# Kernel tuning notes

Hardware: AMD Instinct MI355X
Metric: run time of the kernel (lower is better)

The kernel has to match this reference:

```python
import jax, jax.numpy as jnp
import numpy as np

DIM = 1024
NUM_HEADS = 16
HEAD_DIM = DIM // NUM_HEADS


def setup_inputs() -> dict:
    key = jax.random.key(0)
    k1, k2, k3, k4, k5, k6 = jax.random.split(key, 6)
    B, T, C = 4, 2048, DIM
    s = 1.0 / np.sqrt(C)
    return {
        "x": jax.random.normal(k1, (B, T, C), dtype=jnp.float32),
        "attn_bias": jax.random.normal(k2, (B, T, T), dtype=jnp.float32),
        "qkv_w": jax.random.uniform(k3, (3 * C, C), dtype=jnp.float32, minval=-s, maxval=s),
        "qkv_b": jax.random.uniform(k4, (3 * C,), dtype=jnp.float32, minval=-s, maxval=s),
        "out_w": jax.random.uniform(k5, (C, C), dtype=jnp.float32, minval=-s, maxval=s),
        "out_b": jax.random.uniform(k6, (C,), dtype=jnp.float32, minval=-s, maxval=s),
    }


def reference(x, attn_bias, qkv_w, qkv_b, out_w, out_b):
    B, T, C = x.shape
    H, D = NUM_HEADS, HEAD_DIM
    # fused QKV projection (torch Linear: x @ W^T + b)
    qkv = jnp.einsum('btc,fc->btf', x, qkv_w) + qkv_b  # [B,T,3C]
    q, k, v = jnp.split(qkv, 3, axis=-1)
    q = q.reshape(B, T, H, D).transpose(0, 2, 1, 3)  # [B,H,T,D]
    k = k.reshape(B, T, H, D).transpose(0, 2, 1, 3)
    v = v.reshape(B, T, H, D).transpose(0, 2, 1, 3)
    scores = jnp.einsum('bhtd,bhsd->bhts', q, k) / jnp.sqrt(jnp.float32(D))
    scores = scores + attn_bias[:, None, :, :]  # 3-D bias -> broadcast over heads
    attn = jax.nn.softmax(scores, axis=-1)
    out = jnp.einsum('bhts,bhsd->bhtd', attn, v)  # [B,H,T,D]
    out = out.transpose(0, 2, 1, 3).reshape(B, T, C)
    return jnp.einsum('btc,fc->btf', out, out_w) + out_b
```

## Files before the change

### kernel.cpp

```cpp
#include <hip/hip_runtime.h>

#define BATCH 4
#define SEQ   2048
#define CDIM  1024
#define HEADS 16
#define HDIM  64
#define N3    3072
#define NTOK  8192
#define QKP   2048
#define LOG2E 1.44269504f

typedef __attribute__((ext_vector_type(4))) float    float4v;
typedef __attribute__((ext_vector_type(8))) short    short8;
typedef __attribute__((ext_vector_type(8))) __bf16   bf16x8;
typedef __attribute__((ext_vector_type(4))) _Float16 half4v;
typedef __attribute__((ext_vector_type(2))) _Float16 half2v;

__device__ __forceinline__ unsigned short f2bf(float f) {
    union { float f; unsigned int u; } x; x.f = f;
    unsigned int r = x.u + 0x7fffu + ((x.u >> 16) & 1u);
    return (unsigned short)(r >> 16);
}

__device__ __forceinline__ bf16x8 ld_bf8(const unsigned short* p) {
    short8 s = *(const short8*)p;
    return __builtin_bit_cast(bf16x8, s);
}

__device__ __forceinline__ void glds16(const void* g, void* l) {
    __builtin_amdgcn_global_load_lds(
        (const __attribute__((address_space(1))) void*)g,
        (__attribute__((address_space(3))) void*)l, 16, 0, 0);
}

__global__ void cast_f32_bf16(const float* __restrict__ in,
                              unsigned short* __restrict__ out, int n4) {
    int i = blockIdx.x * blockDim.x + threadIdx.x;
    if (i >= n4) return;
    float4v v = ((const float4v*)in)[i];
    ushort4 r;
    r.x = f2bf(v[0]); r.y = f2bf(v[1]); r.z = f2bf(v[2]); r.w = f2bf(v[3]);
    ((ushort4*)out)[i] = r;
}

__global__ __launch_bounds__(256, 3)
void gemm_bt(const unsigned short* __restrict__ A,
             const unsigned short* __restrict__ Bm,
             const float* __restrict__ bias,
             void* __restrict__ Cout,
             void* __restrict__ Cout2,
             int M, int N, int K, int mode)
{
    __shared__ alignas(16) unsigned short As[128 * 64];
    __shared__ alignas(16) unsigned short Bs[128 * 64];

    const int tid  = threadIdx.x;
    const int lane = tid & 63;
    const int wave = tid >> 6;
    const int wr = wave >> 1, wc = wave & 1;
    const int lm = lane & 15, quad = lane >> 4;
    const size_t m0 = (size_t)blockIdx.y * 128;
    const size_t n0 = (size_t)blockIdx.x * 128;

    const unsigned short* ag[4];
    const unsigned short* bg[4];
    unsigned short* la[4];
    unsigned short* lb[4];
#pragma unroll
    for (int i = 0; i < 4; i++) {
        int idx = tid + i * 256;
        int row = idx >> 3;
        int lc  = (idx & 7) ^ (row & 7);
        ag[i] = &A [(m0 + row) * K + lc * 8];
        bg[i] = &Bm[(n0 + row) * K + lc * 8];
        la[i] = &As[(idx & ~63) * 8];
        lb[i] = &Bs[(idx & ~63) * 8];
    }

    float4v acc[4][4];
#pragma unroll
    for (int i = 0; i < 4; i++)
#pragma unroll
        for (int j = 0; j < 4; j++) acc[i][j] = (float4v){0.f, 0.f, 0.f, 0.f};

    for (int k0 = 0; k0 < K; k0 += 64) {
#pragma unroll
        for (int i = 0; i < 4; i++) glds16(ag[i], la[i]);
#pragma unroll
        for (int i = 0; i < 4; i++) glds16(bg[i], lb[i]);
#pragma unroll
        for (int i = 0; i < 4; i++) { ag[i] += 64; bg[i] += 64; }
        __syncthreads();
#pragma unroll
        for (int kk = 0; kk < 2; kk++) {
            bf16x8 af[4], bfr[4];
#pragma unroll
            for (int t = 0; t < 4; t++) {
                int slot = ((quad + kk * 4) ^ (lm & 7)) * 8;
                af [t] = ld_bf8(&As[(wr * 64 + t * 16 + lm) * 64 + slot]);
                bfr[t] = ld_bf8(&Bs[(wc * 64 + t * 16 + lm) * 64 + slot]);
            }
#pragma unroll
            for (int ti = 0; ti < 4; ti++)
#pragma unroll
                for (int tj = 0; tj < 4; tj++)
                    acc[ti][tj] = __builtin_amdgcn_mfma_f32_16x16x32_bf16(
                        af[ti], bfr[tj], acc[ti][tj], 0, 0, 0);
        }
        __syncthreads();
    }

#pragma unroll
    for (int ti = 0; ti < 4; ti++) {
        size_t row = m0 + wr * 64 + ti * 16 + quad * 4;
#pragma unroll
        for (int tj = 0; tj < 4; tj++) {
            int col = (int)n0 + wc * 64 + tj * 16 + lm;
            float bv = bias[col];
            if (mode == 0) {
#pragma unroll
                for (int r = 0; r < 4; r++)
                    ((float*)Cout)[(row + r) * N + col] = acc[ti][tj][r] + bv;
            } else if (col < 2 * CDIM) {
#pragma unroll
                for (int r = 0; r < 4; r++)
                    ((unsigned short*)Cout)[(row + r) * QKP + col] =
                        f2bf(acc[ti][tj][r] + bv);
            } else {
                int hd = col - 2 * CDIM;
                int bb = (int)(row >> 11);
                int s  = (int)(row & 2047);
                half4v hv;
#pragma unroll
                for (int r = 0; r < 4; r++) hv[r] = (_Float16)(acc[ti][tj][r] + bv);
                *(half4v*)((unsigned short*)Cout2 +
                           ((size_t)bb * CDIM + hd) * SEQ + s) = hv;
            }
        }
    }
}

__global__ __launch_bounds__(256, 4)
void attn_kernel(const unsigned short* __restrict__ qk,
                 const unsigned short* __restrict__ vT,
                 const float* __restrict__ bias,
                 unsigned short* __restrict__ outp)
{
    __shared__ alignas(16) char smem[32768];
    float*          BiasS = (float*)smem;
    unsigned short* Qs    = (unsigned short*)smem;
    unsigned short* Ks    = (unsigned short*)(smem + 16384);
    unsigned short* Vts   = (unsigned short*)(smem + 24576);

    const int tid  = threadIdx.x;
    const int lane = tid & 63, wave = tid >> 6;
    const int lm = lane & 15, quad = lane >> 4;
    const int q0 = blockIdx.x * 64;
    const int bh = blockIdx.y;
    const int bb = bh >> 4, h = bh & 15;
    const size_t rowbase = (size_t)bb * SEQ;
    const unsigned short* vTh = vT + (size_t)bh * HDIM * SEQ;
    const float* biasb = bias + (size_t)bb * SEQ * SEQ + (size_t)q0 * SEQ;

#pragma unroll
    for (int i = 0; i < 2; i++) {
        int idx = tid + i * 256;
        int row = idx >> 3;
        int lc  = (idx & 7) ^ (row & 7);
        glds16(&qk[(rowbase + q0 + row) * QKP + h * 64 + lc * 8], &Qs[(idx & ~63) * 8]);
    }
    __syncthreads();
    bf16x8 bq[2];
#pragma unroll
    for (int kk = 0; kk < 2; kk++)
        bq[kk] = ld_bf8(&Qs[(wave * 16 + lm) * 64 + (((quad + kk * 4) ^ (lm & 7)) * 8)]);

    const unsigned short *kg0, *kg1, *vg0, *vg1;
    unsigned short *lk0, *lk1, *lv0, *lv1;
    {
        int idx = tid, row = idx >> 3, lc = (idx & 7) ^ (row & 7);
        kg0 = &qk[(rowbase + row) * QKP + CDIM + h * 64 + lc * 8];
        vg0 = &vTh[(size_t)row * SEQ + lc * 8];
        lk0 = &Ks[(idx & ~63) * 8];
        lv0 = &Vts[(idx & ~63) * 8];
        idx = tid + 256; row = idx >> 3; lc = (idx & 7) ^ (row & 7);
        kg1 = &qk[(rowbase + row) * QKP + CDIM + h * 64 + lc * 8];
        vg1 = &vTh[(size_t)row * SEQ + lc * 8];
        lk1 = &Ks[(idx & ~63) * 8];
        lv1 = &Vts[(idx & ~63) * 8];
    }
    const float* bgp[4];
    float*       lbp[4];
#pragma unroll
    for (int i = 0; i < 4; i++) {
        int idx = tid + i * 256;
        int row = idx >> 4;
        int lc  = (idx & 15) ^ (row & 15);
        bgp[i] = &biasb[(size_t)row * SEQ + lc * 4];
        lbp[i] = &BiasS[(idx & ~63) * 4];
    }

    float rsum = 0.f;
    float4v o[4];
#pragma unroll
    for (int t = 0; t < 4; t++) o[t] = (float4v){0.f, 0.f, 0.f, 0.f};

    for (int it = 0; it < SEQ / 64; ++it) {
        __syncthreads();
        glds16(kg0, lk0); glds16(kg1, lk1);
        glds16(vg0, lv0); glds16(vg1, lv1);
#pragma unroll
        for (int i = 0; i < 4; i++) glds16(bgp[i], lbp[i]);
        kg0 += 64 * QKP; kg1 += 64 * QKP;
        vg0 += 64; vg1 += 64;
#pragma unroll
        for (int i = 0; i < 4; i++) bgp[i] += 64;
        __syncthreads();

        float4v st[4];
#pragma unroll
        for (int tj = 0; tj < 4; tj++) {
            bf16x8 ak0 = ld_bf8(&Ks[(tj * 16 + lm) * 64 + (((quad    ) ^ (lm & 7)) * 8)]);
            bf16x8 ak1 = ld_bf8(&Ks[(tj * 16 + lm) * 64 + (((quad + 4) ^ (lm & 7)) * 8)]);
            st[tj] = (float4v){0.f, 0.f, 0.f, 0.f};
            st[tj] = __builtin_amdgcn_mfma_f32_16x16x32_bf16(ak0, bq[0], st[tj], 0, 0, 0);
            st[tj] = __builtin_amdgcn_mfma_f32_16x16x32_bf16(ak1, bq[1], st[tj], 0, 0, 0);
        }

        half4v pa[4];
#pragma unroll
        for (int tj = 0; tj < 4; tj++) {
            float4v bv = *(const float4v*)&BiasS[(wave * 16 + lm) * 64 +
                                                 (((tj * 4 + quad) ^ lm) * 4)];
            float p[4];
#pragma unroll
            for (int r = 0; r < 4; r++) {
                float sc = fmaf(st[tj][r], 0.125f, bv[r]);
                p[r] = exp2f(sc * LOG2E);
                rsum += p[r];
            }
            half2v plo = __builtin_bit_cast(half2v, __builtin_amdgcn_cvt_pkrtz(p[0], p[1]));
            half2v phi = __builtin_bit_cast(half2v, __builtin_amdgcn_cvt_pkrtz(p[2], p[3]));
            pa[tj][0] = plo[0]; pa[tj][1] = plo[1];
            pa[tj][2] = phi[0]; pa[tj][3] = phi[1];
        }

#pragma unroll
        for (int tj = 0; tj < 4; tj++) {
            int c = tj * 4 + quad;
#pragma unroll
            for (int dt = 0; dt < 4; dt++) {
                int row = dt * 16 + lm;
                int off = (((c >> 1) ^ (lm & 7)) * 8) + (c & 1) * 4;
                half4v vb = *(const half4v*)&Vts[row * 64 + off];
                o[dt] = __builtin_amdgcn_mfma_f32_16x16x16f16(pa[tj], vb, o[dt], 0, 0, 0);
            }
        }
    }

    float l = rsum;
    l += __shfl_xor(l, 16);
    l += __shfl_xor(l, 32);
    float invl = 1.0f / l;
    float i4[4];
#pragma unroll
    for (int r = 0; r < 4; r++) i4[r] = __shfl(invl, quad * 4 + r, 16);
#pragma unroll
    for (int dt = 0; dt < 4; dt++) {
        int col = h * 64 + dt * 16 + lm;
#pragma unroll
        for (int r = 0; r < 4; r++) {
            size_t trow = rowbase + q0 + wave * 16 + quad * 4 + r;
            outp[trow * CDIM + col] = f2bf(o[dt][r] * i4[r]);
        }
    }
}

extern "C" void kernel_launch(void* const* d_in, const int* in_sizes, int n_in,
                              void* d_out, int out_size, void* d_ws, size_t ws_size,
                              hipStream_t stream)
{
    const float* x         = (const float*)d_in[0];
    const float* attn_bias = (const float*)d_in[1];
    const float* qkv_w     = (const float*)d_in[2];
    const float* qkv_b     = (const float*)d_in[3];
    const float* out_w     = (const float*)d_in[4];
    const float* out_b     = (const float*)d_in[5];
    float* out = (float*)d_out;

    char* p = (char*)d_ws;
    unsigned short* x_bf   = (unsigned short*)p; p += (size_t)NTOK * CDIM * 2;
    unsigned short* wq_bf  = (unsigned short*)p; p += (size_t)N3 * CDIM * 2;
    unsigned short* wo_bf  = (unsigned short*)p; p += (size_t)CDIM * CDIM * 2;
    unsigned short* qk_bf  = (unsigned short*)p; p += (size_t)NTOK * QKP * 2;
    unsigned short* vT_f16 = (unsigned short*)p; p += (size_t)BATCH * CDIM * SEQ * 2;
    unsigned short* at_bf  = (unsigned short*)p;

    int n4;
    n4 = NTOK * CDIM / 4;
    cast_f32_bf16<<<(n4 + 255) / 256, 256, 0, stream>>>(x, x_bf, n4);
    n4 = N3 * CDIM / 4;
    cast_f32_bf16<<<(n4 + 255) / 256, 256, 0, stream>>>(qkv_w, wq_bf, n4);
    n4 = CDIM * CDIM / 4;
    cast_f32_bf16<<<(n4 + 255) / 256, 256, 0, stream>>>(out_w, wo_bf, n4);

    gemm_bt<<<dim3(N3 / 128, NTOK / 128), 256, 0, stream>>>(
        x_bf, wq_bf, qkv_b, qk_bf, vT_f16, NTOK, N3, CDIM, 1);

    attn_kernel<<<dim3(SEQ / 64, BATCH * HEADS), 256, 0, stream>>>(
        qk_bf, vT_f16, attn_bias, at_bf);

    gemm_bt<<<dim3(CDIM / 128, NTOK / 128), 256, 0, stream>>>(
        at_bf, wo_bf, out_b, out, nullptr, NTOK, CDIM, CDIM, 0);
}
```

Before: 363.7 us.

## Fold softmax scale into Q, seed MFMA with bias, compute row sums via MFMA

The QKV GEMM epilogue now multiplies Q by scale*log2e, so the attention kernel seeds the QK^T MFMA accumulator with bias*log2e and applies raw exp2 directly to the result. This drops the per-element FMA and multiply. The per-lane scalar row-sum accumulation and the cross-lane shuffles are replaced by an extra MFMA against a ones vector, which yields the row sums already in the output layout. This adds four MFMAs per tile and stores pre-scaled Q in bf16, which changes rounding slightly.

```diff
diff --git a/kernel.cpp b/kernel.cpp
--- a/kernel.cpp
+++ b/kernel.cpp
@@ -9,6 +9,7 @@
 #define NTOK  8192
 #define QKP   2048
 #define LOG2E 1.44269504f
+#define QSC   0.18033688f
 
 typedef __attribute__((ext_vector_type(4))) float    float4v;
 typedef __attribute__((ext_vector_type(8))) short    short8;
@@ -122,10 +123,11 @@
                 for (int r = 0; r < 4; r++)
                     ((float*)Cout)[(row + r) * N + col] = acc[ti][tj][r] + bv;
             } else if (col < 2 * CDIM) {
+                float scl = (col < CDIM) ? QSC : 1.0f;
 #pragma unroll
                 for (int r = 0; r < 4; r++)
                     ((unsigned short*)Cout)[(row + r) * QKP + col] =
-                        f2bf(acc[ti][tj][r] + bv);
+                        f2bf((acc[ti][tj][r] + bv) * scl);
             } else {
                 int hd = col - 2 * CDIM;
                 int bb = (int)(row >> 11);
@@ -200,7 +202,8 @@
         lbp[i] = &BiasS[(idx & ~63) * 4];
     }
 
-    float rsum = 0.f;
+    const half4v vones = {(_Float16)1.f, (_Float16)1.f, (_Float16)1.f, (_Float16)1.f};
+    float4v rs4 = (float4v){0.f, 0.f, 0.f, 0.f};
     float4v o[4];
 #pragma unroll
     for (int t = 0; t < 4; t++) o[t] = (float4v){0.f, 0.f, 0.f, 0.f};
@@ -220,9 +223,11 @@
         float4v st[4];
 #pragma unroll
         for (int tj = 0; tj < 4; tj++) {
+            float4v bv = *(const float4v*)&BiasS[(wave * 16 + lm) * 64 +
+                                                 (((tj * 4 + quad) ^ lm) * 4)];
+            st[tj] = bv * LOG2E;
             bf16x8 ak0 = ld_bf8(&Ks[(tj * 16 + lm) * 64 + (((quad    ) ^ (lm & 7)) * 8)]);
             bf16x8 ak1 = ld_bf8(&Ks[(tj * 16 + lm) * 64 + (((quad + 4) ^ (lm & 7)) * 8)]);
-            st[tj] = (float4v){0.f, 0.f, 0.f, 0.f};
             st[tj] = __builtin_amdgcn_mfma_f32_16x16x32_bf16(ak0, bq[0], st[tj], 0, 0, 0);
             st[tj] = __builtin_amdgcn_mfma_f32_16x16x32_bf16(ak1, bq[1], st[tj], 0, 0, 0);
         }
@@ -230,20 +235,19 @@
         half4v pa[4];
 #pragma unroll
         for (int tj = 0; tj < 4; tj++) {
-            float4v bv = *(const float4v*)&BiasS[(wave * 16 + lm) * 64 +
-                                                 (((tj * 4 + quad) ^ lm) * 4)];
-            float p[4];
-#pragma unroll
-            for (int r = 0; r < 4; r++) {
-                float sc = fmaf(st[tj][r], 0.125f, bv[r]);
-                p[r] = exp2f(sc * LOG2E);
-                rsum += p[r];
-            }
-            half2v plo = __builtin_bit_cast(half2v, __builtin_amdgcn_cvt_pkrtz(p[0], p[1]));
-            half2v phi = __builtin_bit_cast(half2v, __builtin_amdgcn_cvt_pkrtz(p[2], p[3]));
+            float p0 = __builtin_amdgcn_exp2f(st[tj][0]);
+            float p1 = __builtin_amdgcn_exp2f(st[tj][1]);
+            float p2 = __builtin_amdgcn_exp2f(st[tj][2]);
+            float p3 = __builtin_amdgcn_exp2f(st[tj][3]);
+            half2v plo = __builtin_bit_cast(half2v, __builtin_amdgcn_cvt_pkrtz(p0, p1));
+            half2v phi = __builtin_bit_cast(half2v, __builtin_amdgcn_cvt_pkrtz(p2, p3));
             pa[tj][0] = plo[0]; pa[tj][1] = plo[1];
             pa[tj][2] = phi[0]; pa[tj][3] = phi[1];
         }
+
+#pragma unroll
+        for (int tj = 0; tj < 4; tj++)
+            rs4 = __builtin_amdgcn_mfma_f32_16x16x16f16(pa[tj], vones, rs4, 0, 0, 0);
 
 #pragma unroll
         for (int tj = 0; tj < 4; tj++) {
@@ -258,13 +262,9 @@
         }
     }
 
-    float l = rsum;
-    l += __shfl_xor(l, 16);
-    l += __shfl_xor(l, 32);
-    float invl = 1.0f / l;
     float i4[4];
 #pragma unroll
-    for (int r = 0; r < 4; r++) i4[r] = __shfl(invl, quad * 4 + r, 16);
+    for (int r = 0; r < 4; r++) i4[r] = 1.0f / rs4[r];
 #pragma unroll
     for (int dt = 0; dt < 4; dt++) {
         int col = h * 64 + dt * 16 + lm;
```

Measured after the change: 353.2 us. 1.03x faster.
